# Performance work log

Hardware: AMD Instinct MI355X
Metric: run time of the kernel (lower is better)

Reference implementation:

```python
import jax, jax.numpy as jnp
import numpy as np

# Dimensions
B, T, IN = 8, 64, 6       # batch, timesteps, strain components
G = 256                   # grain_num
H = 32                    # hidden_dim (units)
W = 128                   # quadratic block width
OUT = 3                   # output_dim
DEPTH = 4                 # quadratic block depth
SD = H + IN               # start_dim = units + in_channels = 38
EPS = 1e-15


def setup_inputs() -> dict:
    key = jax.random.key(0)
    ks = jax.random.split(key, 24)
    s = 0.08  # xavier-ish scale for width-128 linears
    d = {
        "x": jax.random.normal(ks[0], (B, T, IN), dtype=jnp.float32),
        "init_ori": jax.random.normal(ks[1], (B, G, 3), dtype=jnp.float32),
        # Quadratic block branch A (modlist1): first layer SD->W, then (DEPTH-1) W->W
        "qbA_W0": jax.random.normal(ks[2], (SD, W)) * s,
        "qbA_b0": jnp.zeros((W,), jnp.float32),
        "qbA_Ws": jax.random.normal(ks[3], (DEPTH - 1, W, W)) * s,
        "qbA_bs": jnp.zeros((DEPTH - 1, W), jnp.float32),
        # Quadratic block branch B (modlist2)
        "qbB_W0": jax.random.normal(ks[4], (SD, W)) * s,
        "qbB_b0": jnp.zeros((W,), jnp.float32),
        "qbB_Ws": jax.random.normal(ks[5], (DEPTH - 1, W, W)) * s,
        "qbB_bs": jnp.zeros((DEPTH - 1, W), jnp.float32),
        # fc_alpha: W -> H ; fc_beta (1-layer DNN): W -> H
        "alpha_W": jax.random.normal(ks[6], (W, H)) * s,
        "alpha_b": jnp.zeros((H,), jnp.float32),
        "beta_W": jax.random.normal(ks[7], (W, H)) * s,
        "beta_b": jnp.zeros((H,), jnp.float32),
        # nn_out DNN: layers = [H, 128, 128, OUT], tanh between hidden layers
        "out_W0": jax.random.normal(ks[8], (H, 128)) * s,
        "out_b0": jnp.zeros((128,), jnp.float32),
        "out_W1": jax.random.normal(ks[9], (128, 128)) * s,
        "out_b1": jnp.zeros((128,), jnp.float32),
        "out_W2": jax.random.normal(ks[10], (128, OUT)) * s,
        "out_b2": jnp.zeros((OUT,), jnp.float32),
    }
    return d


def reference(x, init_ori, qbA_W0, qbA_b0, qbA_Ws, qbA_bs,
              qbB_W0, qbB_b0, qbB_Ws, qbB_bs,
              alpha_W, alpha_b, beta_W, beta_b,
              out_W0, out_b0, out_W1, out_b1, out_W2, out_b2):
    b = x.shape[0]
    # h0 = zeros with first 3 hidden channels set to initial orientations
    h0 = jnp.zeros((b, G, H), x.dtype).at[:, :, :3].set(init_ori)

    def step(h, x_t):  # h: [B,G,H], x_t: [B,IN]
        sn = jnp.linalg.norm(x_t, axis=-1, keepdims=True)          # [B,1]
        xn = x_t / (sn + EPS)                                      # normalized strain direction
        z = jnp.concatenate(
            [jnp.broadcast_to(xn[:, None, :], (b, G, IN)), h], axis=-1)  # [B,G,SD]
        # quadratic block: elementwise product of two linear branches
        a = jnp.tanh(z @ qbA_W0 + qbA_b0)
        c = jnp.tanh(z @ qbB_W0 + qbB_b0)
        z = a * c
        for j in range(DEPTH - 1):
            a = z @ qbA_Ws[j] + qbA_bs[j]
            c = z @ qbB_Ws[j] + qbB_bs[j]
            if j < DEPTH - 2:  # tanh on all but the last quadratic layer
                a = jnp.tanh(a)
                c = jnp.tanh(c)
            z = a * c
        q = jnp.tanh(z)                                            # [B,G,W]
        alpha = jnp.exp(q @ alpha_W + alpha_b)                     # [B,G,H]
        beta = jnp.tanh(q @ beta_W + beta_b)                       # [B,G,H]
        decay = jnp.exp(-alpha * sn[:, :, None])                   # exp(-alpha*||strain||)
        h_new = decay * (h - beta) + beta                          # gated state update
        # nn_out DNN [H,128,128,OUT] with tanh hidden activations
        o = jnp.tanh(h_new @ out_W0 + out_b0)
        o = jnp.tanh(o @ out_W1 + out_b1)
        o = o @ out_W2 + out_b2                                    # [B,G,OUT]
        return h_new, o

    _, outs = jax.lax.scan(step, h0, jnp.swapaxes(x, 0, 1))        # outs: [T,B,G,OUT]
    return jnp.transpose(outs, (1, 2, 0, 3))                       # [B,G,T,OUT]
```

## Files before the change

kernel.cpp:

```cpp
#include <hip/hip_runtime.h>

typedef _Float16 f16;
typedef _Float16 f16x4 __attribute__((ext_vector_type(4)));
typedef _Float16 f16x8 __attribute__((ext_vector_type(8)));
typedef float f32x4 __attribute__((ext_vector_type(4)));
typedef unsigned int u32;

#define MFMA16(a,b,c) __builtin_amdgcn_mfma_f32_16x16x32_f16(a,b,c,0,0,0)

#define BAR() asm volatile("s_waitcnt lgkmcnt(0)\n\ts_barrier" ::: "memory")

#define OFF_A0 0
#define OFF_B0 8192
#define OFF_AW 16384
#define OFF_BW 65536
#define OFF_AL 114688
#define OFF_BE 118784
#define OFF_O0 122880
#define OFF_O1 126976
#define OFF_O2 143360
#define PACK_TOTAL 145408
#define OFF_HH 262144

struct PackSrcs { const float* p[9]; };

__global__ __launch_bounds__(256) void pack_all(PackSrcs ps, f16* __restrict__ dst){
  int idx = blockIdx.x*256 + threadIdx.x;
  if (idx >= PACK_TOTAL) return;
  const float* src; int base, Kreal, Nreal, KT;
  if (idx < 16384){
    if (idx < 8192){ src=ps.p[0]; base=0; } else { src=ps.p[1]; base=8192; }
    Kreal=38; Nreal=128; KT=2;
  } else if (idx < 65536){
    int s=(idx-16384)>>14; src=ps.p[2]+s*16384; base=16384+s*16384; Kreal=128; Nreal=128; KT=4;
  } else if (idx < 114688){
    int s=(idx-65536)>>14; src=ps.p[3]+s*16384; base=65536+s*16384; Kreal=128; Nreal=128; KT=4;
  } else if (idx < 122880){
    if (idx<118784){ src=ps.p[4]; base=114688; } else { src=ps.p[5]; base=118784; }
    Kreal=128; Nreal=32; KT=4;
  } else if (idx < 126976){
    src=ps.p[6]; base=122880; Kreal=32; Nreal=128; KT=1;
  } else if (idx < 143360){
    src=ps.p[7]; base=126976; Kreal=128; Nreal=128; KT=4;
  } else {
    src=ps.p[8]; base=143360; Kreal=128; Nreal=3; KT=4;
  }
  int local = idx - base;
  int j = local & 7, lane = (local>>3)&63, rem = local>>9;
  int kt = rem % KT, nt = rem / KT;
  int k = kt*32 + ((lane>>4)<<3) + j;
  int n = nt*16 + (lane&15);
  if (base < 16384) k = (k < 32) ? (k + 6) : 99;
  dst[idx] = (f16)((k<Kreal && n<Nreal) ? src[k*Nreal+n] : 0.f);
}

__device__ __forceinline__ float tanhfast(float x){
  float e = __builtin_amdgcn_exp2f(x * 2.885390082f);
  return 1.f - 2.f*__builtin_amdgcn_rcpf(e + 1.f);
}
__device__ __forceinline__ float expfast(float x){
  return __builtin_amdgcn_exp2f(x * 1.44269504f);
}

__device__ __forceinline__ f16x8 ldW(const f16* wp, int off, int KT, int nt, int kt, int l){
  return *(const f16x8*)(wp + off + (((nt*KT + kt)*64 + l)<<3));
}

template<int LAST>
__device__ __forceinline__ void qphase(const f16* __restrict__ Zi, f16* __restrict__ Zo,
                                       const f16x8 (&WA)[4], const f16x8 (&WB)[4],
                                       const float* __restrict__ bA,
                                       const float* __restrict__ bB,
                                       int l, int d0, int n16){
  f16x8 Bq[4];
#pragma unroll
  for (int kt=0; kt<4; ++kt) Bq[kt] = *(const f16x8*)(Zi + ((kt*64 + l)<<3));
  f32x4 a = *(const f32x4*)(bA + d0);
  f32x4 c = *(const f32x4*)(bB + d0);
#pragma unroll
  for (int kt=0; kt<4; ++kt){
    a = MFMA16(WA[kt], Bq[kt], a);
    c = MFMA16(WB[kt], Bq[kt], c);
  }
  f16x4 z4;
#pragma unroll
  for (int i=0;i<4;++i){
    float z = LAST ? tanhfast(a[i]*c[i]) : tanhfast(a[i])*tanhfast(c[i]);
    z4[i] = (f16)z;
  }
  int kt_o = d0>>5, lane_o = (((d0&31)>>3)<<4) | n16, j0 = d0&7;
  *(f16x4*)(Zo + ((kt_o*64 + lane_o)<<3) + j0) = z4;
}

__global__ __launch_bounds__(512,2)
void lmsc_rec(const float* __restrict__ x, const float* __restrict__ init_ori,
              const f16* __restrict__ wp,
              const float* __restrict__ w0Araw, const float* __restrict__ w0Braw,
              const float* __restrict__ ba0, const float* __restrict__ bas,
              const float* __restrict__ bb0, const float* __restrict__ bbs,
              const float* __restrict__ b_al, const float* __restrict__ b_be,
              f16* __restrict__ hG)
{
  __shared__ __align__(16) f16 S[2][512];
  __shared__ __align__(16) f16 Z[2][2048];
  __shared__ float biasA[4][128], biasB[4][128], biasAB[64];
  __shared__ float hbuf[512];
  __shared__ float xnL[64][8];
  __shared__ __align__(16) float UA[64][128];
  __shared__ __align__(16) float UC[64][128];

  const int tid = (int)threadIdx.x;
  const int l = tid & 63, wid = tid >> 6;
  const int n16 = l & 15, rhi = l >> 4;
  const int d0 = (wid<<4) + (rhi<<2);
  const int tile = (int)blockIdx.x, b = tile >> 4, Rbase = tile << 4;

  f16x8 w0A = ldW(wp, OFF_A0, 2, wid, 0, l);
  f16x8 w0B = ldW(wp, OFF_B0, 2, wid, 0, l);
  f16x8 wqA[3][4], wqB[3][4];
#pragma unroll
  for (int ly=0;ly<3;++ly)
#pragma unroll
    for (int kt=0;kt<4;++kt){
      wqA[ly][kt] = ldW(wp, OFF_AW + ly*16384, 4, wid, kt, l);
      wqB[ly][kt] = ldW(wp, OFF_BW + ly*16384, 4, wid, kt, l);
    }
  f16x8 wal[4], wbe[4];
  if (wid < 2){
#pragma unroll
    for (int kt=0;kt<4;++kt){
      wal[kt] = ldW(wp, OFF_AL, 4, wid, kt, l);
      wbe[kt] = ldW(wp, OFF_BE, 4, wid, kt, l);
    }
  }

  if (tid < 128){
    biasA[0][tid] = ba0[tid]; biasB[0][tid] = bb0[tid];
#pragma unroll
    for (int j=0;j<3;++j){ biasA[1+j][tid] = bas[j*128+tid]; biasB[1+j][tid] = bbs[j*128+tid]; }
  }
  if (tid < 32){ biasAB[tid] = b_al[tid]; biasAB[32+tid] = b_be[tid]; }
  if (tid < 64){
    const float* xp = x + (b*64 + tid)*6;
    float s2 = 0.f;
#pragma unroll
    for (int i=0;i<6;++i) s2 += xp[i]*xp[i];
    float sn = sqrtf(s2);
    float inv = 1.f/(sn + 1e-15f);
#pragma unroll
    for (int i=0;i<6;++i) xnL[tid][i] = xp[i]*inv;
    xnL[tid][6] = sn;
  }
  __syncthreads();
  {
    const int dim = tid & 127, t0 = (tid >> 7) << 4;
    float wA[6], wC[6];
#pragma unroll
    for (int k=0;k<6;++k){ wA[k] = w0Araw[k*128+dim]; wC[k] = w0Braw[k*128+dim]; }
    const float bA_ = biasA[0][dim], bC_ = biasB[0][dim];
#pragma unroll
    for (int tt=0;tt<16;++tt){
      int t = t0 + tt;
      float aA = bA_, aC = bC_;
#pragma unroll
      for (int k=0;k<6;++k){
        float xv = xnL[t][k];
        aA += xv * wA[k];
        aC += xv * wC[k];
      }
      UA[t][dim] = aA; UC[t][dim] = aC;
    }
  }
  if (tid < 256){
    int r = tid & 15, cc = tid >> 4;
#pragma unroll
    for (int e=0;e<2;++e){
      int c = cc + e*16;
      float h0 = (c < 3) ? init_ori[(Rbase + r)*3 + c] : 0.f;
      hbuf[c*16 + r] = h0;
      f16 hh = (f16)h0, hl = (f16)(h0 - (float)hh);
      int idx = ((((c>>3)<<4) | r)<<3) + (c&7);
      S[0][idx] = hh; S[1][idx] = hl;
    }
  }
  __syncthreads();

  for (int t=0; t<64; ++t){
    {
      f16x8 Bh = *(const f16x8*)(&S[0][l<<3]);
      f16x8 Bl = *(const f16x8*)(&S[1][l<<3]);
      f32x4 aH = *(const f32x4*)(&UA[t][d0]);
      f32x4 cH = *(const f32x4*)(&UC[t][d0]);
      f32x4 aL = {0,0,0,0}, cL = {0,0,0,0};
      aH = MFMA16(w0A, Bh, aH); aL = MFMA16(w0A, Bl, aL);
      cH = MFMA16(w0B, Bh, cH); cL = MFMA16(w0B, Bl, cL);
      f16x4 z4;
#pragma unroll
      for (int i=0;i<4;++i)
        z4[i] = (f16)(tanhfast(aH[i]+aL[i]) * tanhfast(cH[i]+cL[i]));
      int kt_o = d0>>5, lane_o = (((d0&31)>>3)<<4) | n16, j0 = d0&7;
      *(f16x4*)(&Z[0][((kt_o*64 + lane_o)<<3) + j0]) = z4;
    }
    BAR();
    qphase<0>(Z[0], Z[1], wqA[0], wqB[0], biasA[1], biasB[1], l, d0, n16);
    BAR();
    qphase<0>(Z[1], Z[0], wqA[1], wqB[1], biasA[2], biasB[2], l, d0, n16);
    BAR();
    qphase<1>(Z[0], Z[1], wqA[2], wqB[2], biasA[3], biasB[3], l, d0, n16);
    BAR();
    if (wid < 2){
      f16x8 q[4];
#pragma unroll
      for (int kt=0;kt<4;++kt) q[kt] = *(const f16x8*)(&Z[1][(kt*64+l)<<3]);
      f32x4 ua = *(const f32x4*)(&biasAB[d0]);
      f32x4 ub = *(const f32x4*)(&biasAB[32+d0]);
#pragma unroll
      for (int kt=0;kt<4;++kt){
        ua = MFMA16(wal[kt], q[kt], ua);
        ub = MFMA16(wbe[kt], q[kt], ub);
      }
      float sn = xnL[t][6];
      int mt = tile*64 + t;
      f16x4 hh4, hl4;
#pragma unroll
      for (int i=0;i<4;++i){
        float alv = expfast(fminf(ua[i], 80.f));
        float bev = tanhfast(ub[i]);
        int c = d0 + i;
        float hold = hbuf[c*16 + n16];
        float hn = __builtin_amdgcn_exp2f(-1.44269504f*alv*sn)*(hold - bev) + bev;
        hbuf[c*16 + n16] = hn;
        f16 hh = (f16)hn; hh4[i] = hh; hl4[i] = (f16)(hn - (float)hh);
      }
      if (t < 63){
        int sb = ((((d0>>3)<<4) | n16)<<3) + (d0&7);
        *(f16x4*)(&S[0][sb]) = hh4;
        *(f16x4*)(&S[1][sb]) = hl4;
      }
      int lane_o = ((d0>>3)<<4) | n16;
      *(f16x4*)(hG + mt*512 + lane_o*8 + (d0&7)) = hh4;
    }
    BAR();
  }
}

__global__ __launch_bounds__(512,4)
void lmsc_out(const f16* __restrict__ wp, const f16* __restrict__ hG,
              const float* __restrict__ bo0, const float* __restrict__ bo1,
              const float* __restrict__ bo2, float* __restrict__ out)
{
  __shared__ __align__(16) f16 o1b[16384];
  __shared__ __align__(16) f16 o2b[16384];
  const int tid=(int)threadIdx.x, l=tid&63, wid=tid>>6;
  const int n16=l&15, rhi=l>>4;
  const int mtb = (int)blockIdx.x * 8;
  f16x8 W0a = ldW(wp, OFF_O0, 1, wid, 0, l);
  f16x8 W1a[4], W2a[4];
#pragma unroll
  for (int kt=0;kt<4;++kt){ W1a[kt]=ldW(wp,OFF_O1,4,wid,kt,l); W2a[kt]=ldW(wp,OFF_O2,4,0,kt,l); }
  const int d0 = wid*16 + rhi*4;
  const f32x4 b0v = *(const f32x4*)(bo0 + d0);
  const f32x4 b1v = *(const f32x4*)(bo1 + d0);
  const int kt_o = d0>>5, lane_o = (((d0&31)>>3)<<4) + n16, j0 = d0&7;
#pragma unroll
  for (int s=0;s<8;++s){
    int mt = mtb + s;
    f16x8 Bh = *(const f16x8*)(hG + ((mt*64+l)<<3));
    f32x4 acc = b0v;
    acc = MFMA16(W0a, Bh, acc);
    f16x4 z4;
#pragma unroll
    for (int i=0;i<4;++i) z4[i] = (f16)tanhfast(acc[i]);
    *(f16x4*)(&o1b[(((s*4+kt_o)*64 + lane_o)<<3) + j0]) = z4;
  }
  __syncthreads();
#pragma unroll
  for (int s=0;s<8;++s){
    f32x4 acc = b1v;
#pragma unroll
    for (int kt=0;kt<4;++kt){
      f16x8 B = *(const f16x8*)(&o1b[((s*4+kt)*64 + l)<<3]);
      acc = MFMA16(W1a[kt], B, acc);
    }
    f16x4 z4;
#pragma unroll
    for (int i=0;i<4;++i) z4[i] = (f16)tanhfast(acc[i]);
    *(f16x4*)(&o2b[(((s*4+kt_o)*64 + lane_o)<<3) + j0]) = z4;
  }
  __syncthreads();
  {
    f32x4 acc = {0,0,0,0};
#pragma unroll
    for (int kt=0;kt<4;++kt){
      f16x8 B = *(const f16x8*)(&o2b[((wid*4+kt)*64 + l)<<3]);
      acc = MFMA16(W2a[kt], B, acc);
    }
    if (l < 16){
      int mt = mtb + wid, grow = (mt>>6)*16 + n16, tt = mt & 63;
#pragma unroll
      for (int i=0;i<3;++i)
        out[(grow*64 + tt)*3 + i] = acc[i] + bo2[i];
    }
  }
}

extern "C" void kernel_launch(void* const* d_in, const int* in_sizes, int n_in,
                              void* d_out, int out_size, void* d_ws, size_t ws_size,
                              hipStream_t stream){
  const float* x        = (const float*)d_in[0];
  const float* init_ori = (const float*)d_in[1];
  f16* wp = (f16*)d_ws;

  PackSrcs ps;
  ps.p[0] = (const float*)d_in[2];
  ps.p[1] = (const float*)d_in[6];
  ps.p[2] = (const float*)d_in[4];
  ps.p[3] = (const float*)d_in[8];
  ps.p[4] = (const float*)d_in[10];
  ps.p[5] = (const float*)d_in[12];
  ps.p[6] = (const float*)d_in[14];
  ps.p[7] = (const float*)d_in[16];
  ps.p[8] = (const float*)d_in[18];
  pack_all<<<(PACK_TOTAL+255)/256, 256, 0, stream>>>(ps, wp);

  lmsc_rec<<<128,512,0,stream>>>(x, init_ori, wp,
      (const float*)d_in[2],  (const float*)d_in[6],
      (const float*)d_in[3],  (const float*)d_in[5],
      (const float*)d_in[7],  (const float*)d_in[9],
      (const float*)d_in[11], (const float*)d_in[13],
      wp + OFF_HH);
  lmsc_out<<<1024,512,0,stream>>>(wp, wp + OFF_HH,
      (const float*)d_in[15], (const float*)d_in[17], (const float*)d_in[19],
      (float*)d_out);
}
```

Measured before the change: 135.6 us.

## Halve recurrent block to 4 waves, each computing two output tiles

The recurrent kernel now launches 256 threads per block instead of 512. Each wave computes two 16-row output tiles per quadratic layer, holding twice as many weight fragments in registers. The hidden state moves from shared memory into per-thread registers. The goal is cheaper barriers and more MFMA work per wave on the serial time loop, at the cost of much higher register pressure and possible spills under launch_bounds(256,1).

```diff
diff --git a/kernel.cpp b/kernel.cpp
--- a/kernel.cpp
+++ b/kernel.cpp
@@ -67,32 +67,41 @@
 }
 
 template<int LAST>
-__device__ __forceinline__ void qphase(const f16* __restrict__ Zi, f16* __restrict__ Zo,
-                                       const f16x8 (&WA)[4], const f16x8 (&WB)[4],
-                                       const float* __restrict__ bA,
-                                       const float* __restrict__ bB,
-                                       int l, int d0, int n16){
+__device__ __forceinline__ void qphase2(const f16* __restrict__ Zi, f16* __restrict__ Zo,
+                                        const f16x8 (&WA)[2][4], const f16x8 (&WB)[2][4],
+                                        const float* __restrict__ bA,
+                                        const float* __restrict__ bB,
+                                        int l, int d0q, int n16){
   f16x8 Bq[4];
 #pragma unroll
   for (int kt=0; kt<4; ++kt) Bq[kt] = *(const f16x8*)(Zi + ((kt*64 + l)<<3));
-  f32x4 a = *(const f32x4*)(bA + d0);
-  f32x4 c = *(const f32x4*)(bB + d0);
+  f32x4 a0 = *(const f32x4*)(bA + d0q);
+  f32x4 c0 = *(const f32x4*)(bB + d0q);
+  f32x4 a1 = *(const f32x4*)(bA + d0q + 16);
+  f32x4 c1 = *(const f32x4*)(bB + d0q + 16);
 #pragma unroll
   for (int kt=0; kt<4; ++kt){
-    a = MFMA16(WA[kt], Bq[kt], a);
-    c = MFMA16(WB[kt], Bq[kt], c);
-  }
-  f16x4 z4;
-#pragma unroll
-  for (int i=0;i<4;++i){
-    float z = LAST ? tanhfast(a[i]*c[i]) : tanhfast(a[i])*tanhfast(c[i]);
-    z4[i] = (f16)z;
-  }
-  int kt_o = d0>>5, lane_o = (((d0&31)>>3)<<4) | n16, j0 = d0&7;
-  *(f16x4*)(Zo + ((kt_o*64 + lane_o)<<3) + j0) = z4;
-}
-
-__global__ __launch_bounds__(512,2)
+    a0 = MFMA16(WA[0][kt], Bq[kt], a0);
+    c0 = MFMA16(WB[0][kt], Bq[kt], c0);
+    a1 = MFMA16(WA[1][kt], Bq[kt], a1);
+    c1 = MFMA16(WB[1][kt], Bq[kt], c1);
+  }
+#pragma unroll
+  for (int s=0; s<2; ++s){
+    f32x4 a = s ? a1 : a0, c = s ? c1 : c0;
+    f16x4 z4;
+#pragma unroll
+    for (int i=0;i<4;++i){
+      float z = LAST ? tanhfast(a[i]*c[i]) : tanhfast(a[i])*tanhfast(c[i]);
+      z4[i] = (f16)z;
+    }
+    int d0s = d0q + 16*s;
+    int kt_o = d0s>>5, lane_o = (((d0s&31)>>3)<<4) | n16, j0 = d0s&7;
+    *(f16x4*)(Zo + ((kt_o*64 + lane_o)<<3) + j0) = z4;
+  }
+}
+
+__global__ __launch_bounds__(256,1)
 void lmsc_rec(const float* __restrict__ x, const float* __restrict__ init_ori,
               const f16* __restrict__ wp,
               const float* __restrict__ w0Araw, const float* __restrict__ w0Braw,
@@ -104,7 +113,6 @@
   __shared__ __align__(16) f16 S[2][512];
   __shared__ __align__(16) f16 Z[2][2048];
   __shared__ float biasA[4][128], biasB[4][128], biasAB[64];
-  __shared__ float hbuf[512];
   __shared__ float xnL[64][8];
   __shared__ __align__(16) float UA[64][128];
   __shared__ __align__(16) float UC[64][128];
@@ -112,19 +120,26 @@
   const int tid = (int)threadIdx.x;
   const int l = tid & 63, wid = tid >> 6;
   const int n16 = l & 15, rhi = l >> 4;
-  const int d0 = (wid<<4) + (rhi<<2);
+  const int d0q = (wid<<5) + (rhi<<2);
+  const int d0p = (wid<<4) + (rhi<<2);
   const int tile = (int)blockIdx.x, b = tile >> 4, Rbase = tile << 4;
 
-  f16x8 w0A = ldW(wp, OFF_A0, 2, wid, 0, l);
-  f16x8 w0B = ldW(wp, OFF_B0, 2, wid, 0, l);
-  f16x8 wqA[3][4], wqB[3][4];
+  f16x8 w0A[2], w0B[2];
+#pragma unroll
+  for (int s=0;s<2;++s){
+    w0A[s] = ldW(wp, OFF_A0, 2, wid*2+s, 0, l);
+    w0B[s] = ldW(wp, OFF_B0, 2, wid*2+s, 0, l);
+  }
+  f16x8 wqA[3][2][4], wqB[3][2][4];
 #pragma unroll
   for (int ly=0;ly<3;++ly)
 #pragma unroll
-    for (int kt=0;kt<4;++kt){
-      wqA[ly][kt] = ldW(wp, OFF_AW + ly*16384, 4, wid, kt, l);
-      wqB[ly][kt] = ldW(wp, OFF_BW + ly*16384, 4, wid, kt, l);
-    }
+    for (int s=0;s<2;++s)
+#pragma unroll
+      for (int kt=0;kt<4;++kt){
+        wqA[ly][s][kt] = ldW(wp, OFF_AW + ly*16384, 4, wid*2+s, kt, l);
+        wqB[ly][s][kt] = ldW(wp, OFF_BW + ly*16384, 4, wid*2+s, kt, l);
+      }
   f16x8 wal[4], wbe[4];
   if (wid < 2){
 #pragma unroll
@@ -151,15 +166,22 @@
     for (int i=0;i<6;++i) xnL[tid][i] = xp[i]*inv;
     xnL[tid][6] = sn;
   }
+  float hreg[4] = {0.f,0.f,0.f,0.f};
+  if (wid < 2){
+#pragma unroll
+    for (int i=0;i<4;++i){
+      int c = d0p + i;
+      hreg[i] = (c < 3) ? init_ori[(Rbase + n16)*3 + c] : 0.f;
+    }
+  }
   __syncthreads();
   {
-    const int dim = tid & 127, t0 = (tid >> 7) << 4;
+    const int dim = tid & 127, t0 = (tid >> 7) << 5;
     float wA[6], wC[6];
 #pragma unroll
     for (int k=0;k<6;++k){ wA[k] = w0Araw[k*128+dim]; wC[k] = w0Braw[k*128+dim]; }
     const float bA_ = biasA[0][dim], bC_ = biasB[0][dim];
-#pragma unroll
-    for (int tt=0;tt<16;++tt){
+    for (int tt=0;tt<32;++tt){
       int t = t0 + tt;
       float aA = bA_, aC = bC_;
 #pragma unroll
@@ -171,13 +193,12 @@
       UA[t][dim] = aA; UC[t][dim] = aC;
     }
   }
-  if (tid < 256){
+  {
     int r = tid & 15, cc = tid >> 4;
 #pragma unroll
     for (int e=0;e<2;++e){
       int c = cc + e*16;
       float h0 = (c < 3) ? init_ori[(Rbase + r)*3 + c] : 0.f;
-      hbuf[c*16 + r] = h0;
       f16 hh = (f16)h0, hl = (f16)(h0 - (float)hh);
       int idx = ((((c>>3)<<4) | r)<<3) + (c&7);
       S[0][idx] = hh; S[1][idx] = hl;
@@ -189,31 +210,41 @@
     {
       f16x8 Bh = *(const f16x8*)(&S[0][l<<3]);
       f16x8 Bl = *(const f16x8*)(&S[1][l<<3]);
-      f32x4 aH = *(const f32x4*)(&UA[t][d0]);
-      f32x4 cH = *(const f32x4*)(&UC[t][d0]);
-      f32x4 aL = {0,0,0,0}, cL = {0,0,0,0};
-      aH = MFMA16(w0A, Bh, aH); aL = MFMA16(w0A, Bl, aL);
-      cH = MFMA16(w0B, Bh, cH); cL = MFMA16(w0B, Bl, cL);
-      f16x4 z4;
-#pragma unroll
-      for (int i=0;i<4;++i)
-        z4[i] = (f16)(tanhfast(aH[i]+aL[i]) * tanhfast(cH[i]+cL[i]));
-      int kt_o = d0>>5, lane_o = (((d0&31)>>3)<<4) | n16, j0 = d0&7;
-      *(f16x4*)(&Z[0][((kt_o*64 + lane_o)<<3) + j0]) = z4;
-    }
-    BAR();
-    qphase<0>(Z[0], Z[1], wqA[0], wqB[0], biasA[1], biasB[1], l, d0, n16);
-    BAR();
-    qphase<0>(Z[1], Z[0], wqA[1], wqB[1], biasA[2], biasB[2], l, d0, n16);
-    BAR();
-    qphase<1>(Z[0], Z[1], wqA[2], wqB[2], biasA[3], biasB[3], l, d0, n16);
+      f32x4 aH0 = *(const f32x4*)(&UA[t][d0q]);
+      f32x4 cH0 = *(const f32x4*)(&UC[t][d0q]);
+      f32x4 aH1 = *(const f32x4*)(&UA[t][d0q+16]);
+      f32x4 cH1 = *(const f32x4*)(&UC[t][d0q+16]);
+      f32x4 aL0 = {0,0,0,0}, cL0 = {0,0,0,0}, aL1 = {0,0,0,0}, cL1 = {0,0,0,0};
+      aH0 = MFMA16(w0A[0], Bh, aH0); cH0 = MFMA16(w0B[0], Bh, cH0);
+      aH1 = MFMA16(w0A[1], Bh, aH1); cH1 = MFMA16(w0B[1], Bh, cH1);
+      aL0 = MFMA16(w0A[0], Bl, aL0); cL0 = MFMA16(w0B[0], Bl, cL0);
+      aL1 = MFMA16(w0A[1], Bl, aL1); cL1 = MFMA16(w0B[1], Bl, cL1);
+#pragma unroll
+      for (int s=0;s<2;++s){
+        f32x4 aH = s ? aH1 : aH0, aL = s ? aL1 : aL0;
+        f32x4 cH = s ? cH1 : cH0, cL = s ? cL1 : cL0;
+        f16x4 z4;
+#pragma unroll
+        for (int i=0;i<4;++i)
+          z4[i] = (f16)(tanhfast(aH[i]+aL[i]) * tanhfast(cH[i]+cL[i]));
+        int d0s = d0q + 16*s;
+        int kt_o = d0s>>5, lane_o = (((d0s&31)>>3)<<4) | n16, j0 = d0s&7;
+        *(f16x4*)(&Z[0][((kt_o*64 + lane_o)<<3) + j0]) = z4;
+      }
+    }
+    BAR();
+    qphase2<0>(Z[0], Z[1], wqA[0], wqB[0], biasA[1], biasB[1], l, d0q, n16);
+    BAR();
+    qphase2<0>(Z[1], Z[0], wqA[1], wqB[1], biasA[2], biasB[2], l, d0q, n16);
+    BAR();
+    qphase2<1>(Z[0], Z[1], wqA[2], wqB[2], biasA[3], biasB[3], l, d0q, n16);
     BAR();
     if (wid < 2){
       f16x8 q[4];
 #pragma unroll
       for (int kt=0;kt<4;++kt) q[kt] = *(const f16x8*)(&Z[1][(kt*64+l)<<3]);
-      f32x4 ua = *(const f32x4*)(&biasAB[d0]);
-      f32x4 ub = *(const f32x4*)(&biasAB[32+d0]);
+      f32x4 ua = *(const f32x4*)(&biasAB[d0p]);
+      f32x4 ub = *(const f32x4*)(&biasAB[32+d0p]);
 #pragma unroll
       for (int kt=0;kt<4;++kt){
         ua = MFMA16(wal[kt], q[kt], ua);
@@ -226,19 +257,17 @@
       for (int i=0;i<4;++i){
         float alv = expfast(fminf(ua[i], 80.f));
         float bev = tanhfast(ub[i]);
-        int c = d0 + i;
-        float hold = hbuf[c*16 + n16];
-        float hn = __builtin_amdgcn_exp2f(-1.44269504f*alv*sn)*(hold - bev) + bev;
-        hbuf[c*16 + n16] = hn;
+        float hn = __builtin_amdgcn_exp2f(-1.44269504f*alv*sn)*(hreg[i] - bev) + bev;
+        hreg[i] = hn;
         f16 hh = (f16)hn; hh4[i] = hh; hl4[i] = (f16)(hn - (float)hh);
       }
       if (t < 63){
-        int sb = ((((d0>>3)<<4) | n16)<<3) + (d0&7);
+        int sb = ((((d0p>>3)<<4) | n16)<<3) + (d0p&7);
         *(f16x4*)(&S[0][sb]) = hh4;
         *(f16x4*)(&S[1][sb]) = hl4;
       }
-      int lane_o = ((d0>>3)<<4) | n16;
-      *(f16x4*)(hG + mt*512 + lane_o*8 + (d0&7)) = hh4;
+      int lane_o = ((d0p>>3)<<4) | n16;
+      *(f16x4*)(hG + mt*512 + lane_o*8 + (d0p&7)) = hh4;
     }
     BAR();
   }
@@ -323,7 +352,7 @@
   ps.p[8] = (const float*)d_in[18];
   pack_all<<<(PACK_TOTAL+255)/256, 256, 0, stream>>>(ps, wp);
 
-  lmsc_rec<<<128,512,0,stream>>>(x, init_ori, wp,
+  lmsc_rec<<<128,256,0,stream>>>(x, init_ori, wp,
       (const float*)d_in[2],  (const float*)d_in[6],
       (const float*)d_in[3],  (const float*)d_in[5],
       (const float*)d_in[7],  (const float*)d_in[9],
```

Result: slower. 157.8 us (+16.4%).
